# Performance work log

Hardware: AMD Instinct MI355X
Metric: run time of the kernel (lower is better)

The kernel has to match this reference:

```python
import jax, jax.numpy as jnp
import numpy as np

B = 64        # BATCH_SIZE
C_IN = 16
L = 8192
FFT0 = 64
FFT1 = 256
CO = 32       # c_out per fft branch (c_out=64 / 2 ffts)
RATIO = FFT1 // FFT0  # 4
EPS = 1e-5


def setup_inputs() -> dict:
    key = jax.random.key(0)
    ks = jax.random.split(key, 12)
    x = jax.random.normal(ks[0], (B, C_IN, L), jnp.float32)
    bn_gamma = 1.0 + 0.1 * jax.random.normal(ks[1], (2, B), jnp.float32)
    bn_beta = 0.1 * jax.random.normal(ks[2], (2, B), jnp.float32)
    mk_r = 0.1 * jax.random.normal(ks[3], (RATIO, RATIO), jnp.float32)
    mk_i = 0.1 * jax.random.normal(ks[4], (RATIO, RATIO), jnp.float32)
    mb_r = 0.1 * jax.random.normal(ks[5], (RATIO,), jnp.float32)
    mb_i = 0.1 * jax.random.normal(ks[6], (RATIO,), jnp.float32)
    fk0_r = 0.1 * jax.random.normal(ks[7], (FFT0 // 2 + 1, C_IN, CO), jnp.float32)
    fk0_i = 0.1 * jax.random.normal(ks[8], (FFT0 // 2 + 1, C_IN, CO), jnp.float32)
    fk1_r = 0.1 * jax.random.normal(ks[9], (FFT1 // 2 + 1, C_IN, CO), jnp.float32)
    fk1_i = 0.1 * jax.random.normal(ks[10], (FFT1 // 2 + 1, C_IN, CO), jnp.float32)
    pbias = 0.1 * jax.random.normal(ks[11], (2 * CO,), jnp.float32)
    return dict(x=x, bn_gamma=bn_gamma, bn_beta=bn_beta, mk_r=mk_r, mk_i=mk_i,
                mb_r=mb_r, mb_i=mb_i, fk0_r=fk0_r, fk0_i=fk0_i,
                fk1_r=fk1_r, fk1_i=fk1_i, pbias=pbias)


def _stft(x2d, n):
    # torch.stft(center=True, pad_mode='reflect', hop=n_fft, rect window),
    # then keep onesided bins and drop the last frame (as in the module).
    N = x2d.shape[0]
    xp = jnp.pad(x2d, ((0, 0), (n // 2, n // 2)), mode='reflect')
    frames = xp.reshape(N, -1, n)               # (N, T+1, n), hop == n_fft
    spec = jnp.fft.rfft(frames, axis=-1)        # onesided == [:, :, :n//2+1]
    return spec[:, :-1, :]                      # drop last frame -> (N, T, n//2+1)


def _zero_interp(p, ratio, out_f):
    # interleave (ratio-1) zeros along the freq axis, then crop to out_f bins
    b, t, f, c = p.shape
    z = jnp.zeros((b, t, f, ratio - 1, c), p.dtype)
    q = jnp.concatenate([p[:, :, :, None, :], z], axis=3).reshape(b, t, f * ratio, c)
    return q[:, :, :out_f, :]


def _cbn(xc, g, b):
    # BatchNorm2d(BATCH_SIZE) after permute(3,0,1,2): channel dim == batch dim,
    # stats over (c_in, T, F) per batch element; complex mean, |.|^2 variance.
    mu = jnp.mean(xc, axis=(1, 2, 3), keepdims=True)
    d = xc - mu
    var = jnp.mean((d * jnp.conj(d)).real, axis=(1, 2, 3), keepdims=True)
    xh = d / jnp.sqrt(var + EPS)
    return xh * g[:, None, None, None] + b[:, None, None, None]


def _istft(out, n):
    # out: (B, T, F, CO) complex. Mirrors permute/reshape + frame repeat + istft
    # (hop=n_fft, rect window, center=True -> trim n//2 on both ends).
    Bq, T, F, Co = out.shape
    pf = out.transpose(0, 3, 2, 1).reshape(Bq * Co, F, T)
    pf = jnp.concatenate([pf, pf[:, :, :1]], axis=-1)   # append copy of frame 0 -> T+1 frames
    fr = jnp.fft.irfft(pf, n=n, axis=1)                 # (N, n, T+1)
    sig = fr.transpose(0, 2, 1).reshape(Bq * Co, -1)    # overlap-add trivial (hop=n)
    sig = sig[:, n // 2: n // 2 + T * n]                # length L
    return sig.reshape(Bq, Co, -1).transpose(0, 2, 1)   # (B, L, CO)


def _forward(x, bn_gamma, bn_beta, mk_r, mk_i, mb_r, mb_i,
             fk0_r, fk0_i, fk1_r, fk1_i, pbias):
    x2 = x.reshape(B * C_IN, L)

    def spec(n):
        s = _stft(x2, n)                                 # (B*C_IN, T, n//2+1)
        T = s.shape[1]
        return s.reshape(B, C_IN, T, n // 2 + 1).transpose(0, 2, 3, 1)  # (B,T,F,C_IN)

    p0 = spec(FFT0)   # (B, 128, 33, 16)
    p1 = spec(FFT1)   # (B, 32, 129, 16)

    # attention merge across time (small fft -> large fft scale)
    pm = p0.reshape(B, -1, RATIO, FFT0 // 2 + 1, C_IN).transpose(0, 1, 3, 4, 2)  # (B,T1,F0,C,r)
    kc = mk_r + 1j * mk_i
    att = jnp.einsum('btfcr,rs->btfcs', pm, kc) + (mb_r + 1j * mb_i)
    a = jax.nn.softmax(jnp.abs(att), axis=-1)            # real weights (complex(a,0) in torch)
    merged = jnp.sum(pm * a, axis=-1) * float(RATIO)     # (B, T1, F0, C_IN)

    F1 = FFT1 // 2 + 1
    mask01 = _zero_interp(jnp.ones(merged.shape, jnp.float32), RATIO, F1)
    up = _zero_interp(merged, RATIO, F1)

    acc0 = p0                                            # own-scale mask is all ones
    acc1 = mask01 * up + (1.0 - mask01) * p1             # cross-scale + complementary mask

    def head(acc, g, b, fkr, fki, n):
        xbn = _cbn(acc, g, b)
        out = jnp.einsum('btfi,fio->btfo', xbn, fkr + 1j * fki)  # FILTER_FLAG merge
        return _istft(out, n)

    t0 = head(acc0, bn_gamma[0], bn_beta[0], fk0_r, fk0_i, FFT0)  # (B, L, CO)
    t1 = head(acc1, bn_gamma[1], bn_beta[1], fk1_r, fk1_i, FFT1)  # (B, L, CO)

    y = jnp.concatenate([t0, t1], axis=2) + pbias        # + patch_bias.real
    y = jax.nn.relu(y)                                   # ACT_DOMAIN == 'time'
    return y.transpose(0, 2, 1)                          # (B, c_out, L)


def reference(x, bn_gamma, bn_beta, mk_r, mk_i, mb_r, mb_i,
              fk0_r, fk0_i, fk1_r, fk1_i, pbias):
    return _forward(x, bn_gamma, bn_beta, mk_r, mk_i, mb_r, mb_i,
                    fk0_r, fk0_i, fk1_r, fk1_i, pbias)
```

## Files before the change

### kernel.cpp

```cpp
#include <hip/hip_runtime.h>
#include <math.h>

#define BB   64
#define CIN  16
#define LL   8192
#define CO   32
#define TCO  64
constexpr int T0n = 128;
constexpr int T1n = 32;
constexpr int F0n = 33;
constexpr int F1n = 129;
constexpr int PW0 = 48;
constexpr int PW1 = 144;

typedef unsigned int   uint32;
typedef unsigned short u16;
typedef __attribute__((ext_vector_type(8))) _Float16 half8;
typedef __attribute__((ext_vector_type(4))) float    f32x4;
typedef __attribute__((ext_vector_type(4))) uint32   u32x4;

__device__ inline int imin(int a, int b) { return a < b ? a : b; }

__device__ inline uint32 pack2h(float a, float b) {
    _Float16 ha = (_Float16)a, hb = (_Float16)b;
    return ((uint32)(*(u16*)&hb) << 16) | (uint32)(*(u16*)&ha);
}

__device__ inline half8 flip_pm(half8 v) {
    u32x4 u;
    __builtin_memcpy(&u, &v, 16);
    u.y ^= 0x80008000u;
    u.w ^= 0x80008000u;
    half8 r;
    __builtin_memcpy(&r, &u, 16);
    return r;
}

template<int N, int F, int TFR, int NTILES, int KTT, int MT_W, int NT_W,
         int NT_STRIDE, bool MT_SPLIT>
__global__ __launch_bounds__(256)
void stft_mfma_kernel(const float* __restrict__ x,
                      const u16* __restrict__ dhi, const u16* __restrict__ dlo,
                      float* __restrict__ p) {
    constexpr int PADN = N + 8;
    __shared__ __align__(16) u16 Xhi[TFR * PADN];
    __shared__ __align__(16) u16 Xlo[TFR * PADN];
    int bc = blockIdx.x;
    const float* xrow = x + (size_t)bc * LL;

    for (int i = threadIdx.x; i < N / 2; i += 256) {
        float v = xrow[N / 2 - i];
        _Float16 h = (_Float16)v;
        Xhi[i] = *(u16*)&h;
        _Float16 l = (_Float16)(v - (float)h);
        Xlo[i] = *(u16*)&l;
    }
    for (int i4 = N / 8 + threadIdx.x; i4 < TFR * N / 4; i4 += 256) {
        int i = 4 * i4;
        int row = i / N, colk = i - row * N;
        float4 v = *(const float4*)&xrow[i - N / 2];
        _Float16 h0 = (_Float16)v.x, h1 = (_Float16)v.y,
                 h2 = (_Float16)v.z, h3 = (_Float16)v.w;
        uint2 hv, lv;
        hv.x = ((uint32)(*(u16*)&h1) << 16) | (uint32)(*(u16*)&h0);
        hv.y = ((uint32)(*(u16*)&h3) << 16) | (uint32)(*(u16*)&h2);
        lv.x = pack2h(v.x - (float)h0, v.y - (float)h1);
        lv.y = pack2h(v.z - (float)h2, v.w - (float)h3);
        *(uint2*)&Xhi[row * PADN + colk] = hv;
        *(uint2*)&Xlo[row * PADN + colk] = lv;
    }
    __syncthreads();

    int lane = threadIdx.x & 63, w = threadIdx.x >> 6;
    int col = lane & 15, quad = lane >> 4;
    f32x4 acc[MT_W][NT_W];
    #pragma unroll
    for (int mi = 0; mi < MT_W; ++mi)
        #pragma unroll
        for (int nj = 0; nj < NT_W; ++nj) {
            f32x4 z = {0.f, 0.f, 0.f, 0.f};
            acc[mi][nj] = z;
        }

    for (int kt = 0; kt < KTT; ++kt) {
        half8 ah[MT_W], al[MT_W];
        #pragma unroll
        for (int mi = 0; mi < MT_W; ++mi) {
            int mt = MT_SPLIT ? (w * MT_W + mi) : mi;
            int t  = mt * 16 + col;
            ah[mi] = *(const half8*)&Xhi[t * PADN + kt * 32 + quad * 8];
            al[mi] = *(const half8*)&Xlo[t * PADN + kt * 32 + quad * 8];
        }
        #pragma unroll
        for (int nj = 0; nj < NT_W; ++nj) {
            int nt = MT_SPLIT ? nj : (w + nj * NT_STRIDE);
            if (nt < NTILES) {
                half8 bh = ((const half8*)dhi)[(nt * KTT + kt) * 64 + lane];
                half8 bl = ((const half8*)dlo)[(nt * KTT + kt) * 64 + lane];
                #pragma unroll
                for (int mi = 0; mi < MT_W; ++mi) {
                    acc[mi][nj] = __builtin_amdgcn_mfma_f32_16x16x32_f16(ah[mi], bh, acc[mi][nj], 0, 0, 0);
                    acc[mi][nj] = __builtin_amdgcn_mfma_f32_16x16x32_f16(ah[mi], bl, acc[mi][nj], 0, 0, 0);
                    acc[mi][nj] = __builtin_amdgcn_mfma_f32_16x16x32_f16(al[mi], bh, acc[mi][nj], 0, 0, 0);
                }
            }
        }
    }

    int b = bc / CIN, c = bc % CIN;
    #pragma unroll
    for (int mi = 0; mi < MT_W; ++mi) {
        int mt = MT_SPLIT ? (w * MT_W + mi) : mi;
        #pragma unroll
        for (int nj = 0; nj < NT_W; ++nj) {
            int nt = MT_SPLIT ? nj : (w + nj * NT_STRIDE);
            if (nt < NTILES) {
                int j = nt * 16 + col;
                if (j < 2 * F) {
                    int t0 = mt * 16 + quad * 4;
                    f32x4 a = acc[mi][nj];
                    #pragma unroll
                    for (int r = 0; r < 4; ++r) {
                        p[(((size_t)b * TFR + t0 + r) * CIN + c) * (2 * F) + j] = a[r];
                    }
                }
            }
        }
    }
}

__global__ __launch_bounds__(256)
void init_d_kernel(u16* __restrict__ dhi0, u16* __restrict__ dlo0,
                   u16* __restrict__ dhi1, u16* __restrict__ dlo1) {
    int idx = blockIdx.x * 256 + threadIdx.x;
    constexpr int SZ0 = 5 * 2 * 64 * 8;
    constexpr int SZ1 = 17 * 8 * 64 * 8;
    int N, F, KTT, id; u16 *dh, *dl;
    if (idx < SZ0)            { N = 64;  F = F0n; KTT = 2; dh = dhi0; dl = dlo0; id = idx; }
    else if (idx < SZ0 + SZ1) { N = 256; F = F1n; KTT = 8; dh = dhi1; dl = dlo1; id = idx - SZ0; }
    else return;
    int jj   = id & 7;
    int lane = (id >> 3) & 63;
    int rest = id >> 9;
    int kt   = rest % KTT;
    int nt   = rest / KTT;
    int j = nt * 16 + (lane & 15);
    int k = kt * 32 + (lane >> 4) * 8 + jj;
    float v = 0.f;
    if (j < 2 * F) {
        int f = j >> 1;
        int u = (f * k) % N;
        double th = 6.283185307179586476925286766559 * (double)u / (double)N;
        v = (float)((j & 1) ? -sin(th) : cos(th));
    }
    _Float16 h = (_Float16)v;
    _Float16 l = (_Float16)(v - (float)h);
    dh[id] = *(u16*)&h;
    dl[id] = *(u16*)&l;
}

__global__ __launch_bounds__(256)
void merge_kernel(const float2* __restrict__ p0, float2* __restrict__ p1,
                  const float* __restrict__ mkr, const float* __restrict__ mki,
                  const float* __restrict__ mbr, const float* __restrict__ mbi) {
    int idx = blockIdx.x * 256 + threadIdx.x;
    const int total = BB * T1n * CIN * F0n;
    if (idx >= total) return;
    int f0 = idx % F0n; int r1 = idx / F0n;
    int c  = r1 % CIN;  int r2 = r1 / CIN;
    int t1 = r2 % T1n;  int b  = r2 / T1n;
    float2 pm[4];
    #pragma unroll
    for (int r = 0; r < 4; ++r) {
        int t = t1 * 4 + r;
        pm[r] = p0[(((size_t)b * T0n + t) * CIN + c) * F0n + f0];
    }
    float mag[4], mx = -1e30f;
    #pragma unroll
    for (int s = 0; s < 4; ++s) {
        float atr = mbr[s], ati = mbi[s];
        #pragma unroll
        for (int r = 0; r < 4; ++r) {
            float kr = mkr[r * 4 + s], ki = mki[r * 4 + s];
            atr = fmaf(pm[r].x, kr, atr); atr = fmaf(-pm[r].y, ki, atr);
            ati = fmaf(pm[r].x, ki, ati); ati = fmaf(pm[r].y, kr, ati);
        }
        mag[s] = sqrtf(atr * atr + ati * ati);
        mx = fmaxf(mx, mag[s]);
    }
    float se = 0.f;
    #pragma unroll
    for (int s = 0; s < 4; ++s) { mag[s] = expf(mag[s] - mx); se += mag[s]; }
    float inv = 4.0f / se;
    float mr = 0.f, mi = 0.f;
    #pragma unroll
    for (int r = 0; r < 4; ++r) { mr = fmaf(pm[r].x, mag[r], mr); mi = fmaf(pm[r].y, mag[r], mi); }
    p1[(((size_t)b * T1n + t1) * CIN + c) * F1n + 4 * f0] = make_float2(mr * inv, mi * inv);
}

__global__ __launch_bounds__(256)
void cbn_partial_kernel(const float2* __restrict__ p0, const float2* __restrict__ p1,
                        float4* __restrict__ part) {
    int blk  = blockIdx.x;
    int c8   = blk & 7;
    int b    = (blk >> 3) & 63;
    int head = blk >> 9;
    int Nel  = head ? (T1n * CIN * F1n) : (T0n * CIN * F0n);
    const float2* base = head ? (p1 + (size_t)b * (T1n * CIN * F1n))
                              : (p0 + (size_t)b * (T0n * CIN * F0n));
    int chunk = (Nel + 7) / 8;
    int i0 = c8 * chunk, i1 = imin(i0 + chunk, Nel);
    float sr = 0.f, si = 0.f, s2 = 0.f;
    for (int i = i0 + threadIdx.x; i < i1; i += 256) {
        float2 v = base[i];
        sr += v.x; si += v.y;
        s2 = fmaf(v.x, v.x, s2); s2 = fmaf(v.y, v.y, s2);
    }
    __shared__ float red[3][256];
    red[0][threadIdx.x] = sr; red[1][threadIdx.x] = si; red[2][threadIdx.x] = s2;
    __syncthreads();
    for (int off = 128; off > 0; off >>= 1) {
        if (threadIdx.x < off) {
            red[0][threadIdx.x] += red[0][threadIdx.x + off];
            red[1][threadIdx.x] += red[1][threadIdx.x + off];
            red[2][threadIdx.x] += red[2][threadIdx.x + off];
        }
        __syncthreads();
    }
    if (threadIdx.x == 0)
        part[blk] = make_float4(red[0][0], red[1][0], red[2][0], 0.f);
}

__global__ __launch_bounds__(128)
void cbn_final_kernel(const float4* __restrict__ part,
                      const float* __restrict__ gamma, const float* __restrict__ beta,
                      float4* __restrict__ bn) {
    int hb = threadIdx.x;
    float sr = 0.f, si = 0.f, s2 = 0.f;
    #pragma unroll
    for (int c = 0; c < 8; ++c) {
        float4 v = part[hb * 8 + c];
        sr += v.x; si += v.y; s2 += v.z;
    }
    int head = hb >> 6;
    int Nel  = head ? (T1n * CIN * F1n) : (T0n * CIN * F0n);
    float invN = 1.f / (float)Nel;
    float mur = sr * invN, mui = si * invN;
    float var = s2 * invN - mur * mur - mui * mui;
    float g = gamma[hb] * rsqrtf(var + 1e-5f);
    bn[hb] = make_float4(g, beta[hb] - mur * g, -mui * g, 0.f);
}

__global__ __launch_bounds__(256)
void init_w_kernel(u16* __restrict__ whi0, u16* __restrict__ wlo0,
                   u16* __restrict__ whi1, u16* __restrict__ wlo1) {
    int idx = blockIdx.x * 256 + threadIdx.x;
    constexpr int SZ0 = 2 * 3 * 64 * 8;
    constexpr int SZ1 = 8 * 9 * 64 * 8;
    int N, F, KT, id; u16 *dh, *dl;
    if (idx < SZ0)            { N = 64;  F = F0n; KT = 3; dh = whi0; dl = wlo0; id = idx; }
    else if (idx < SZ0 + SZ1) { N = 256; F = F1n; KT = 9; dh = whi1; dl = wlo1; id = idx - SZ0; }
    else return;
    int j    = id & 7;
    int lane = (id >> 3) & 63;
    int rest = id >> 9;
    int kt   = rest % KT;
    int mt   = rest / KT;
    int m  = mt * 16 + (lane & 15);
    int k2 = kt * 32 + (lane >> 4) * 8 + j;
    float v = 0.f;
    if (k2 < 2 * F) {
        int f = k2 >> 1;
        double scale = (f == 0 || f == F - 1) ? (1024.0 / N) : (2048.0 / N);
        int u = (m * f) % N;
        double th = 6.283185307179586476925286766559 * (double)u / (double)N;
        v = (float)((k2 & 1) ? (-scale * sin(th)) : (scale * cos(th)));
    }
    _Float16 h = (_Float16)v;
    _Float16 l = (_Float16)(v - (float)h);
    dh[id] = *(u16*)&h;
    dl[id] = *(u16*)&l;
}

__global__ __launch_bounds__(256)
void init_fk_kernel(const float* __restrict__ r0, const float* __restrict__ i0,
                    const float* __restrict__ r1, const float* __restrict__ i1,
                    float4* __restrict__ q0, float4* __restrict__ q1,
                    float2* __restrict__ s0, float2* __restrict__ s1) {
    int idx = blockIdx.x * 256 + threadIdx.x;
    constexpr int NQ0 = 8 * F0n * 32;
    constexpr int NQ1 = 8 * F1n * 32;
    constexpr int NS0 = F0n * 32;
    constexpr int NS1 = F1n * 32;
    if (idx < NQ0) {
        int id = idx;
        int c2 = id / (F0n * 32); int rem = id % (F0n * 32);
        int o = rem / F0n, f = rem % F0n;
        int s = (f * CIN + 2 * c2) * CO + o;
        q0[id] = make_float4(r0[s], i0[s], r0[s + CO], i0[s + CO]);
    } else if (idx < NQ0 + NQ1) {
        int id = idx - NQ0;
        int c2 = id / (F1n * 32); int rem = id % (F1n * 32);
        int o = rem / F1n, f = rem % F1n;
        int s = (f * CIN + 2 * c2) * CO + o;
        q1[id] = make_float4(r1[s], i1[s], r1[s + CO], i1[s + CO]);
    } else if (idx < NQ0 + NQ1 + NS0) {
        int id = idx - NQ0 - NQ1;
        int o = id / F0n, f = id % F0n;
        float sr = 0.f, si = 0.f;
        for (int ci = 0; ci < CIN; ++ci) {
            int s = (f * CIN + ci) * CO + o;
            sr += r0[s]; si += i0[s];
        }
        s0[id] = make_float2(sr, si);
    } else if (idx < NQ0 + NQ1 + NS0 + NS1) {
        int id = idx - NQ0 - NQ1 - NS0;
        int o = id / F1n, f = id % F1n;
        float sr = 0.f, si = 0.f;
        for (int ci = 0; ci < CIN; ++ci) {
            int s = (f * CIN + ci) * CO + o;
            sr += r1[s]; si += i1[s];
        }
        s1[id] = make_float2(sr, si);
    }
}

template<int F, int TFR, int CH0, int PADW>
__global__ __launch_bounds__(256)
void einsum_kernel(const float2* __restrict__ p, const float4* __restrict__ fkq,
                   const float2* __restrict__ fks, const float4* __restrict__ bn,
                   uint32* __restrict__ Ghi, uint32* __restrict__ Glo) {
    constexpr int FCH = 8, TCH = 16;
    constexpr int FCO  = F * 32;
    constexpr int NFCH = PADW / FCH;
    constexpr int NTC  = TFR / TCH;
    __shared__ float2 xs[TCH][CIN][FCH];
    int blk  = blockIdx.x;
    int fch  = blk % NFCH;
    int rest = blk / NFCH;
    int tc   = rest % NTC;
    int b    = rest / NTC;
    int t0   = tc * TCH;
    int f0   = fch * FCH;
    int o    = threadIdx.x >> 3;
    int fl   = threadIdx.x & 7;
    int f    = f0 + fl;
    bool valid = f < F;
    int fc = valid ? f : F - 1;
    float4 kk[8];
    #pragma unroll
    for (int c2 = 0; c2 < 8; ++c2) kk[c2] = fkq[c2 * FCO + o * F + fc];
    float2 fv = fks[o * F + fc];
    float4 par = bn[(CH0 ? 1 : 0) * BB + b];
    float base_re = fmaf(par.y, fv.x, -par.z * fv.y);
    float base_im = fmaf(par.y, fv.y,  par.z * fv.x);

    const float2* pb = p + (size_t)(b * TFR + t0) * CIN * F;
    for (int i = threadIdx.x; i < TCH * CIN * FCH; i += 256) {
        int fi = i & 7;
        int r  = i >> 3;
        int ff = f0 + fi;
        ((float2*)xs)[i] = (ff < F) ? pb[(size_t)r * F + ff] : make_float2(0.f, 0.f);
    }
    __syncthreads();
    for (int tp = 0; tp < TCH; ++tp) {
        float re = 0.f, im = 0.f;
        #pragma unroll
        for (int c2 = 0; c2 < 8; ++c2) {
            float2 xa = xs[tp][2 * c2][fl];
            float2 xb = xs[tp][2 * c2 + 1][fl];
            float4 kkc = kk[c2];
            re = fmaf(xa.x, kkc.x, re); re = fmaf(-xa.y, kkc.y, re);
            im = fmaf(xa.x, kkc.y, im); im = fmaf(xa.y, kkc.x, im);
            re = fmaf(xb.x, kkc.z, re); re = fmaf(-xb.y, kkc.w, re);
            im = fmaf(xb.x, kkc.w, im); im = fmaf(xb.y, kkc.z, im);
        }
        uint32 hv = 0, lv = 0;
        if (valid) {
            float res = fmaf(par.x, re, base_re) * 32.f;
            float ims = fmaf(par.x, im, base_im) * 32.f;
            _Float16 rh = (_Float16)res; _Float16 rl = (_Float16)(res - (float)rh);
            _Float16 ih = (_Float16)ims; _Float16 il = (_Float16)(ims - (float)ih);
            hv = ((uint32)(*(u16*)&ih) << 16) | (uint32)(*(u16*)&rh);
            lv = ((uint32)(*(u16*)&il) << 16) | (uint32)(*(u16*)&rl);
        }
        size_t d = ((size_t)(b * TFR + t0 + tp) * 32 + o) * PADW + f;
        Ghi[d] = hv;
        Glo[d] = lv;
    }
}

template<int N, int F, int TFR, int CH0, int KT, int WMT, bool NTSPLIT>
__device__ __forceinline__ void irfft_body(
        int blk, uint32* bufA,
        const uint32* __restrict__ Ghi, const uint32* __restrict__ Glo,
        const u16* __restrict__ whi, const u16* __restrict__ wlo,
        const float* __restrict__ pbias, float* __restrict__ out) {
    constexpr int PADW = KT * 16;
    constexpr int LDW  = PADW + 4;
    constexpr int R4   = PADW / 4;
    constexpr int WNT  = NTSPLIT ? 1 : 2;
    uint32* bufH = bufA;
    uint32* bufL = bufA + 32 * LDW;
    int t  = blk % (TFR + 1);
    int b  = blk / (TFR + 1);
    int tf = (t == TFR) ? 0 : t;
    const float4* sH = (const float4*)(Ghi + (size_t)(b * TFR + tf) * 32 * PADW);
    const float4* sL = (const float4*)(Glo + (size_t)(b * TFR + tf) * 32 * PADW);
    for (int i = threadIdx.x; i < 32 * R4; i += 256) {
        int row = i / R4, c = i - row * R4;
        *(float4*)&bufH[row * LDW + 4 * c] = sH[i];
        *(float4*)&bufL[row * LDW + 4 * c] = sL[i];
    }
    __syncthreads();

    int lane = threadIdx.x & 63, w = threadIdx.x >> 6;
    int col = lane & 15, quad = lane >> 4;
    const u16* bufh = (const u16*)bufH;
    const u16* bufl = (const u16*)bufL;

    f32x4 accB[WMT][WNT], accD[WMT][WNT];
    #pragma unroll
    for (int mi = 0; mi < WMT; ++mi)
        #pragma unroll
        for (int nj = 0; nj < WNT; ++nj) {
            f32x4 z = {0.f, 0.f, 0.f, 0.f};
            accB[mi][nj] = z; accD[mi][nj] = z;
        }
    for (int kt = 0; kt < KT; ++kt) {
        half8 bh[WNT], bl[WNT], bhm[WNT], blm[WNT];
        #pragma unroll
        for (int nj = 0; nj < WNT; ++nj) {
            int nt = NTSPLIT ? (w & 1) : nj;
            int ro = (nt * 16 + col) * (2 * LDW) + kt * 32 + quad * 8;
            bh[nj]  = *(const half8*)(bufh + ro);
            bl[nj]  = *(const half8*)(bufl + ro);
            bhm[nj] = flip_pm(bh[nj]);
            blm[nj] = flip_pm(bl[nj]);
        }
        #pragma unroll
        for (int mi = 0; mi < WMT; ++mi) {
            int mt = NTSPLIT ? (w >> 1) : (w * WMT + mi);
            half8 ah = ((const half8*)whi)[(mt * KT + kt) * 64 + lane];
            half8 al = ((const half8*)wlo)[(mt * KT + kt) * 64 + lane];
            #pragma unroll
            for (int nj = 0; nj < WNT; ++nj) {
                accB[mi][nj] = __builtin_amdgcn_mfma_f32_16x16x32_f16(ah, bh[nj],  accB[mi][nj], 0, 0, 0);
                accB[mi][nj] = __builtin_amdgcn_mfma_f32_16x16x32_f16(ah, bl[nj],  accB[mi][nj], 0, 0, 0);
                accB[mi][nj] = __builtin_amdgcn_mfma_f32_16x16x32_f16(al, bh[nj],  accB[mi][nj], 0, 0, 0);
                accD[mi][nj] = __builtin_amdgcn_mfma_f32_16x16x32_f16(ah, bhm[nj], accD[mi][nj], 0, 0, 0);
                accD[mi][nj] = __builtin_amdgcn_mfma_f32_16x16x32_f16(ah, blm[nj], accD[mi][nj], 0, 0, 0);
                accD[mi][nj] = __builtin_amdgcn_mfma_f32_16x16x32_f16(al, bhm[nj], accD[mi][nj], 0, 0, 0);
            }
        }
    }
    constexpr float UNSCALE = 1.0f / 32768.0f;
    size_t bb = (size_t)b * TCO;
    #pragma unroll
    for (int mi = 0; mi < WMT; ++mi) {
        int mt = NTSPLIT ? (w >> 1) : (w * WMT + mi);
        #pragma unroll
        for (int hh = 0; hh < 2; ++hh) {
            int m  = mt * 16 + quad * 4 + hh * (N / 2);
            int l0 = t * N + m - N / 2;
            if ((unsigned)l0 < LL) {
                #pragma unroll
                for (int nj = 0; nj < WNT; ++nj) {
                    int nt = NTSPLIT ? (w & 1) : nj;
                    int chn = CH0 + nt * 16 + col;
                    float pb = pbias[chn];
                    f32x4 a = hh ? accD[mi][nj] : accB[mi][nj];
                    float4 v;
                    v.x = fmaxf(fmaf(a[0], UNSCALE, pb), 0.f);
                    v.y = fmaxf(fmaf(a[1], UNSCALE, pb), 0.f);
                    v.z = fmaxf(fmaf(a[2], UNSCALE, pb), 0.f);
                    v.w = fmaxf(fmaf(a[3], UNSCALE, pb), 0.f);
                    *(float4*)(out + (bb + chn) * LL + l0) = v;
                }
            }
        }
    }
}

__global__ __launch_bounds__(256)
void irfft_both_kernel(const uint32* __restrict__ Ghi1, const uint32* __restrict__ Glo1,
                       const uint32* __restrict__ Ghi0, const uint32* __restrict__ Glo0,
                       const u16* __restrict__ whi1, const u16* __restrict__ wlo1,
                       const u16* __restrict__ whi0, const u16* __restrict__ wlo0,
                       const float* __restrict__ pbias, float* __restrict__ out) {
    __shared__ __align__(16) uint32 buf[2 * 32 * (PW1 + 4)];
    constexpr int NB1 = BB * (T1n + 1);
    int blk = blockIdx.x;
    if (blk < NB1)
        irfft_body<256, F1n, T1n, 32, 9, 2, false>(blk, buf, Ghi1, Glo1, whi1, wlo1, pbias, out);
    else
        irfft_body<64, F0n, T0n, 0, 3, 1, true>(blk - NB1, buf, Ghi0, Glo0, whi0, wlo0, pbias, out);
}

extern "C" void kernel_launch(void* const* d_in, const int* in_sizes, int n_in,
                              void* d_out, int out_size, void* d_ws, size_t ws_size,
                              hipStream_t stream) {
    const float* x     = (const float*)d_in[0];
    const float* gam   = (const float*)d_in[1];
    const float* bet   = (const float*)d_in[2];
    const float* mkr   = (const float*)d_in[3];
    const float* mki   = (const float*)d_in[4];
    const float* mbr   = (const float*)d_in[5];
    const float* mbi   = (const float*)d_in[6];
    const float* fk0r  = (const float*)d_in[7];
    const float* fk0i  = (const float*)d_in[8];
    const float* fk1r  = (const float*)d_in[9];
    const float* fk1i  = (const float*)d_in[10];
    const float* pbias = (const float*)d_in[11];
    float* out = (float*)d_out;

    float2* p0   = (float2*)d_ws;
    float2* p1   = p0 + (size_t)BB * T0n * CIN * F0n;
    float4* bnp  = (float4*)(p1 + (size_t)BB * T1n * CIN * F1n);
    float4* part = bnp + 2 * BB;
    float4* fkq0 = part + 1024;
    float4* fkq1 = fkq0 + 8 * F0n * 32;
    float2* fks0 = (float2*)(fkq1 + 8 * F1n * 32);
    float2* fks1 = fks0 + F0n * 32;
    uint32* Ghi1 = (uint32*)(fks1 + F1n * 32);
    uint32* Glo1 = Ghi1 + (size_t)BB * T1n * 32 * PW1;
    uint32* Ghi0 = Glo1 + (size_t)BB * T1n * 32 * PW1;
    uint32* Glo0 = Ghi0 + (size_t)BB * T0n * 32 * PW0;
    u16*    whi0 = (u16*)(Glo0 + (size_t)BB * T0n * 32 * PW0);
    u16*    wlo0 = whi0 + 3072;
    u16*    whi1 = wlo0 + 3072;
    u16*    wlo1 = whi1 + 36864;
    u16*    dhi0 = wlo1 + 36864;
    u16*    dlo0 = dhi0 + 5120;
    u16*    dhi1 = dlo0 + 5120;
    u16*    dlo1 = dhi1 + 69632;

    init_w_kernel<<<(3072 + 36864 + 255) / 256, 256, 0, stream>>>(whi0, wlo0, whi1, wlo1);
    init_d_kernel<<<(5120 + 69632 + 255) / 256, 256, 0, stream>>>(dhi0, dlo0, dhi1, dlo1);
    init_fk_kernel<<<(8 * (F0n + F1n) * 32 + (F0n + F1n) * 32 + 255) / 256, 256, 0, stream>>>(
        fk0r, fk0i, fk1r, fk1i, fkq0, fkq1, fks0, fks1);
    stft_mfma_kernel<64, F0n, 128, 5, 2, 2, 5, 1, true><<<BB * CIN, 256, 0, stream>>>(
        x, dhi0, dlo0, (float*)p0);
    stft_mfma_kernel<256, F1n, 32, 17, 8, 2, 5, 4, false><<<BB * CIN, 256, 0, stream>>>(
        x, dhi1, dlo1, (float*)p1);
    merge_kernel<<<(BB * T1n * CIN * F0n) / 256, 256, 0, stream>>>(p0, p1, mkr, mki, mbr, mbi);
    cbn_partial_kernel<<<1024, 256, 0, stream>>>(p0, p1, part);
    cbn_final_kernel<<<1, 128, 0, stream>>>(part, gam, bet, bnp);
    einsum_kernel<F1n, T1n, 32, PW1><<<(PW1 / 8) * (T1n / 16) * BB, 256, 0, stream>>>(
        p1, fkq1, fks1, bnp, Ghi1, Glo1);
    einsum_kernel<F0n, T0n, 0, PW0><<<(PW0 / 8) * (T0n / 16) * BB, 256, 0, stream>>>(
        p0, fkq0, fks0, bnp, Ghi0, Glo0);
    constexpr int NBI = BB * (T1n + 1) + BB * (T0n + 1);
    irfft_both_kernel<<<NBI, 256, 0, stream>>>(
        Ghi1, Glo1, Ghi0, Glo0, whi1, wlo1, whi0, wlo0, pbias, out);
}
```

Measured before the change: 487.6 us.

## Shrink spectral intermediate padding, swizzle LDS tiles, split irfft per branch

The padded width of the einsum output buffers is reduced (48→40, 144→136), so the einsum writes and irfft reads carry less global traffic. The irfft kernel now zero-fills the missing K columns in LDS and uses an XOR swizzle on the LDS layout instead of row padding, to avoid bank conflicts. The combined irfft kernel is split into two per-branch kernels, each with its own LDS size. This lowers LDS use for the small branch but adds a launch, and the swizzle must line up exactly with the MFMA read pattern.

```diff
diff --git a/kernel.cpp b/kernel.cpp
--- a/kernel.cpp
+++ b/kernel.cpp
@@ -10,8 +10,10 @@
 constexpr int T1n = 32;
 constexpr int F0n = 33;
 constexpr int F1n = 129;
-constexpr int PW0 = 48;
-constexpr int PW1 = 144;
+constexpr int PS0 = 40;
+constexpr int PS1 = 136;
+constexpr int LW0 = 64;
+constexpr int LW1 = 160;
 
 typedef unsigned int   uint32;
 typedef unsigned short u16;
@@ -325,14 +327,14 @@
     }
 }
 
-template<int F, int TFR, int CH0, int PADW>
+template<int F, int TFR, int CH0, int PS>
 __global__ __launch_bounds__(256)
 void einsum_kernel(const float2* __restrict__ p, const float4* __restrict__ fkq,
                    const float2* __restrict__ fks, const float4* __restrict__ bn,
                    uint32* __restrict__ Ghi, uint32* __restrict__ Glo) {
     constexpr int FCH = 8, TCH = 16;
     constexpr int FCO  = F * 32;
-    constexpr int NFCH = PADW / FCH;
+    constexpr int NFCH = PS / FCH;
     constexpr int NTC  = TFR / TCH;
     __shared__ float2 xs[TCH][CIN][FCH];
     int blk  = blockIdx.x;
@@ -384,33 +386,42 @@
             hv = ((uint32)(*(u16*)&ih) << 16) | (uint32)(*(u16*)&rh);
             lv = ((uint32)(*(u16*)&il) << 16) | (uint32)(*(u16*)&rl);
         }
-        size_t d = ((size_t)(b * TFR + t0 + tp) * 32 + o) * PADW + f;
+        size_t d = ((size_t)(b * TFR + t0 + tp) * 32 + o) * PS + f;
         Ghi[d] = hv;
         Glo[d] = lv;
     }
 }
 
-template<int N, int F, int TFR, int CH0, int KT, int WMT, bool NTSPLIT>
-__device__ __forceinline__ void irfft_body(
-        int blk, uint32* bufA,
-        const uint32* __restrict__ Ghi, const uint32* __restrict__ Glo,
-        const u16* __restrict__ whi, const u16* __restrict__ wlo,
-        const float* __restrict__ pbias, float* __restrict__ out) {
-    constexpr int PADW = KT * 16;
-    constexpr int LDW  = PADW + 4;
-    constexpr int R4   = PADW / 4;
-    constexpr int WNT  = NTSPLIT ? 1 : 2;
-    uint32* bufH = bufA;
-    uint32* bufL = bufA + 32 * LDW;
-    int t  = blk % (TFR + 1);
-    int b  = blk / (TFR + 1);
+template<int N, int F, int TFR, int CH0, int KT, int PS, int LDSW, int WMT, bool NTSPLIT>
+__global__ __launch_bounds__(256)
+void irfft_kernel(const uint32* __restrict__ Ghi, const uint32* __restrict__ Glo,
+                  const u16* __restrict__ whi, const u16* __restrict__ wlo,
+                  const float* __restrict__ pbias, float* __restrict__ out) {
+    static_assert(LDSW % 32 == 0 && PS % 4 == 0 && KT * 16 <= LDSW, "geom");
+    constexpr int R4C = PS / 4;
+    constexpr int Z4  = (LDSW - PS) / 4;
+    constexpr int WNT = NTSPLIT ? 1 : 2;
+    __shared__ __align__(16) uint32 buf[2 * 32 * LDSW];
+    uint32* bufH = buf;
+    uint32* bufL = buf + 32 * LDSW;
+
+    int t  = blockIdx.x % (TFR + 1);
+    int b  = blockIdx.x / (TFR + 1);
     int tf = (t == TFR) ? 0 : t;
-    const float4* sH = (const float4*)(Ghi + (size_t)(b * TFR + tf) * 32 * PADW);
-    const float4* sL = (const float4*)(Glo + (size_t)(b * TFR + tf) * 32 * PADW);
-    for (int i = threadIdx.x; i < 32 * R4; i += 256) {
-        int row = i / R4, c = i - row * R4;
-        *(float4*)&bufH[row * LDW + 4 * c] = sH[i];
-        *(float4*)&bufL[row * LDW + 4 * c] = sL[i];
+    const float4* sH = (const float4*)(Ghi + (size_t)(b * TFR + tf) * 32 * PS);
+    const float4* sL = (const float4*)(Glo + (size_t)(b * TFR + tf) * 32 * PS);
+    for (int i = threadIdx.x; i < 32 * R4C; i += 256) {
+        int row = i / R4C, c4 = i - row * R4C;
+        int dst = row * LDSW + ((4 * c4) ^ ((row & 7) * 4));
+        *(float4*)&bufH[dst] = sH[i];
+        *(float4*)&bufL[dst] = sL[i];
+    }
+    for (int i = threadIdx.x; i < 32 * Z4; i += 256) {
+        int row = i / Z4, c4 = R4C + (i - row * Z4);
+        int dst = row * LDSW + ((4 * c4) ^ ((row & 7) * 4));
+        float4 z = make_float4(0.f, 0.f, 0.f, 0.f);
+        *(float4*)&bufH[dst] = z;
+        *(float4*)&bufL[dst] = z;
     }
     __syncthreads();
 
@@ -427,14 +438,16 @@
             f32x4 z = {0.f, 0.f, 0.f, 0.f};
             accB[mi][nj] = z; accD[mi][nj] = z;
         }
+    int swzR = (col & 7) * 8;
     for (int kt = 0; kt < KT; ++kt) {
         half8 bh[WNT], bl[WNT], bhm[WNT], blm[WNT];
         #pragma unroll
         for (int nj = 0; nj < WNT; ++nj) {
             int nt = NTSPLIT ? (w & 1) : nj;
-            int ro = (nt * 16 + col) * (2 * LDW) + kt * 32 + quad * 8;
-            bh[nj]  = *(const half8*)(bufh + ro);
-            bl[nj]  = *(const half8*)(bufl + ro);
+            int R  = nt * 16 + col;
+            int ro = R * (2 * LDSW) + ((kt * 32 + quad * 8) ^ swzR);
+            bh[nj]  = *(const half8*)&bufh[ro];
+            bl[nj]  = *(const half8*)&bufl[ro];
             bhm[nj] = flip_pm(bh[nj]);
             blm[nj] = flip_pm(bl[nj]);
         }
@@ -482,21 +495,6 @@
     }
 }
 
-__global__ __launch_bounds__(256)
-void irfft_both_kernel(const uint32* __restrict__ Ghi1, const uint32* __restrict__ Glo1,
-                       const uint32* __restrict__ Ghi0, const uint32* __restrict__ Glo0,
-                       const u16* __restrict__ whi1, const u16* __restrict__ wlo1,
-                       const u16* __restrict__ whi0, const u16* __restrict__ wlo0,
-                       const float* __restrict__ pbias, float* __restrict__ out) {
-    __shared__ __align__(16) uint32 buf[2 * 32 * (PW1 + 4)];
-    constexpr int NB1 = BB * (T1n + 1);
-    int blk = blockIdx.x;
-    if (blk < NB1)
-        irfft_body<256, F1n, T1n, 32, 9, 2, false>(blk, buf, Ghi1, Glo1, whi1, wlo1, pbias, out);
-    else
-        irfft_body<64, F0n, T0n, 0, 3, 1, true>(blk - NB1, buf, Ghi0, Glo0, whi0, wlo0, pbias, out);
-}
-
 extern "C" void kernel_launch(void* const* d_in, const int* in_sizes, int n_in,
                               void* d_out, int out_size, void* d_ws, size_t ws_size,
                               hipStream_t stream) {
@@ -523,10 +521,10 @@
     float2* fks0 = (float2*)(fkq1 + 8 * F1n * 32);
     float2* fks1 = fks0 + F0n * 32;
     uint32* Ghi1 = (uint32*)(fks1 + F1n * 32);
-    uint32* Glo1 = Ghi1 + (size_t)BB * T1n * 32 * PW1;
-    uint32* Ghi0 = Glo1 + (size_t)BB * T1n * 32 * PW1;
-    uint32* Glo0 = Ghi0 + (size_t)BB * T0n * 32 * PW0;
-    u16*    whi0 = (u16*)(Glo0 + (size_t)BB * T0n * 32 * PW0);
+    uint32* Glo1 = Ghi1 + (size_t)BB * T1n * 32 * PS1;
+    uint32* Ghi0 = Glo1 + (size_t)BB * T1n * 32 * PS1;
+    uint32* Glo0 = Ghi0 + (size_t)BB * T0n * 32 * PS0;
+    u16*    whi0 = (u16*)(Glo0 + (size_t)BB * T0n * 32 * PS0);
     u16*    wlo0 = whi0 + 3072;
     u16*    whi1 = wlo0 + 3072;
     u16*    wlo1 = whi1 + 36864;
@@ -546,11 +544,12 @@
     merge_kernel<<<(BB * T1n * CIN * F0n) / 256, 256, 0, stream>>>(p0, p1, mkr, mki, mbr, mbi);
     cbn_partial_kernel<<<1024, 256, 0, stream>>>(p0, p1, part);
     cbn_final_kernel<<<1, 128, 0, stream>>>(part, gam, bet, bnp);
-    einsum_kernel<F1n, T1n, 32, PW1><<<(PW1 / 8) * (T1n / 16) * BB, 256, 0, stream>>>(
+    einsum_kernel<F1n, T1n, 32, PS1><<<(PS1 / 8) * (T1n / 16) * BB, 256, 0, stream>>>(
         p1, fkq1, fks1, bnp, Ghi1, Glo1);
-    einsum_kernel<F0n, T0n, 0, PW0><<<(PW0 / 8) * (T0n / 16) * BB, 256, 0, stream>>>(
+    irfft_kernel<256, F1n, T1n, 32, 9, PS1, LW1, 2, false><<<BB * (T1n + 1), 256, 0, stream>>>(
+        Ghi1, Glo1, whi1, wlo1, pbias, out);
+    einsum_kernel<F0n, T0n, 0, PS0><<<(PS0 / 8) * (T0n / 16) * BB, 256, 0, stream>>>(
         p0, fkq0, fks0, bnp, Ghi0, Glo0);
-    constexpr int NBI = BB * (T1n + 1) + BB * (T0n + 1);
-    irfft_both_kernel<<<NBI, 256, 0, stream>>>(
-        Ghi1, Glo1, Ghi0, Glo0, whi1, wlo1, whi0, wlo0, pbias, out);
-}
+    irfft_kernel<64, F0n, T0n, 0, 3, PS0, LW0, 1, true><<<BB * (T0n + 1), 256, 0, stream>>>(
+        Ghi0, Glo0, whi0, wlo0, pbias, out);
+}
```

After: 460.9 us. -5.5%, faster.
